# Kernel optimization log

Hardware: AMD Instinct MI355X
Metric: run time of the kernel (lower is better)

The kernel has to match this reference:

```python
import jax, jax.numpy as jnp
import numpy as np

B, C, FRAMES, E, W = 8, 2, 3999, 512, 16
STEP = W // 2  # frame_step = W//2 = 8


def setup_inputs() -> dict:
    key = jax.random.key(0)
    k1, k2 = jax.random.split(key)
    dec_input = jax.random.normal(k1, (B, C, FRAMES, E), dtype=jnp.float32)
    weight = jax.random.normal(k2, (W, E), dtype=jnp.float32) * (1.0 / np.sqrt(E))
    return {"dec_input": dec_input, "weight": weight}


def overlap_and_add(signal, frame_step):
    # signal: [..., frames, frame_length] -> [..., (frames-1)*step + frame_length]
    frames, frame_length = signal.shape[-2], signal.shape[-1]
    output_size = frame_step * (frames - 1) + frame_length
    # target sample index of every element of `signal`
    idx = (jnp.arange(frames)[:, None] * frame_step
           + jnp.arange(frame_length)[None, :]).reshape(-1)  # [frames*frame_length]
    flat = signal.reshape(*signal.shape[:-2], frames * frame_length)
    out = jnp.zeros((*signal.shape[:-2], output_size), dtype=signal.dtype)
    # scatter-accumulate overlapping frames along the last axis
    return out.at[..., idx].add(flat)


def reference(dec_input, weight):
    # dec_input: [B, C, frames, E]; weight: [W, E] (nn.Linear(E, W, bias=False))
    est_source = jnp.einsum('bcle,we->bclw', dec_input, weight)  # [B, C, frames, W]
    return overlap_and_add(est_source, STEP)  # [B, C, T]
```

## Files before the change

kernel.cpp:

```cpp
#include <hip/hip_runtime.h>
#include <cstdint>
#include <cstddef>


#define NBC     16
#define FRAMES  3999
#define EE      512
#define TOUT    32000
#define NGROUP  4000
#define GPB     63

__global__ __launch_bounds__(256, 4) void decoder_kernel(
    const float* __restrict__ dec,
    const float* __restrict__ wgt,
    float* __restrict__ out)
{
    __shared__ float smem[16 * EE];
    float* wl  = smem;
    float* red = smem;

    const int tid   = threadIdx.x;
    const int bc    = blockIdx.x >> 6;
    const int chunk = blockIdx.x & 63;
    const int g0    = chunk * GPB;

    {
        const float4* ws = (const float4*)wgt;
        float4*       wd = (float4*)wl;
        #pragma unroll
        for (int i = 0; i < 8; ++i)
            wd[tid + 256 * i] = ws[tid + 256 * i];
    }
    __syncthreads();

    const int s = tid & 63;
    const int q = tid >> 6;
    const int f = g0 - 1 + s;
    const float vmask = (f >= 0 && f < FRAMES) ? 1.0f : 0.0f;
    const int fr = min(max(f, 0), FRAMES - 1);

    const float* arow = dec + ((size_t)bc * FRAMES + fr) * EE + q * 128;
    const float* wbase = wl + q * 128;

    float acc[16];
    #pragma unroll
    for (int w = 0; w < 16; ++w) acc[w] = 0.f;

    #pragma unroll
    for (int c = 0; c < 8; ++c) {
        float4 xv[4];
        #pragma unroll
        for (int u = 0; u < 4; ++u)
            xv[u] = *(const float4*)(arow + c * 16 + 4 * u);

        #pragma unroll
        for (int w = 0; w < 16; ++w) {
            const float4* wrow = (const float4*)(wbase + w * EE + c * 16);
            float sum = 0.f;
            #pragma unroll
            for (int u = 0; u < 4; ++u) {
                const float4 wq = wrow[u];
                sum += xv[u].x * wq.x + xv[u].y * wq.y
                     + xv[u].z * wq.z + xv[u].w * wq.w;
            }
            acc[w] += sum;
        }
    }

    __syncthreads();
    #pragma unroll
    for (int w = 0; w < 16; ++w)
        red[(q * 16 + w) * 64 + s] = acc[w] * vmask;
    __syncthreads();

    for (int o = tid; o < GPB * 8; o += 256) {
        const int j = o >> 3;
        const int i = o & 7;
        const int g = g0 + j;
        if (g < NGROUP) {
            float v = 0.f;
            #pragma unroll
            for (int qq = 0; qq < 4; ++qq)
                v += red[(qq * 16 + i) * 64 + (j + 1)]
                   + red[(qq * 16 + 8 + i) * 64 + j];
            out[(size_t)bc * TOUT + g * 8 + i] = v;
        }
    }
}

extern "C" void kernel_launch(void* const* d_in, const int* in_sizes, int n_in,
                              void* d_out, int out_size, void* d_ws, size_t ws_size,
                              hipStream_t stream) {
    const float* dec = (const float*)d_in[0];
    const float* wgt = (const float*)d_in[1];
    float* out = (float*)d_out;

    decoder_kernel<<<dim3(1024), dim3(256), 0, stream>>>(dec, wgt, out);
}
```

Measured before the change: 197.5 us.

## Read weights via wave-uniform scalar loads and double-buffer activation loads

Drops the weight copy into shared memory and its barrier. Each wave's weight row offset is made uniform with readfirstlane, so weights can be fetched by scalar loads straight from global memory. Activation float4 loads are double-buffered one chunk ahead to overlap with the FMAs, and the per-row partial sums are folded straight into the accumulators. This cuts LDS traffic and one barrier, but relies on the compiler issuing scalar loads and adds register pressure from the extra buffer.

```diff
diff --git a/kernel.cpp b/kernel.cpp
--- a/kernel.cpp
+++ b/kernel.cpp
@@ -15,59 +15,55 @@
     const float* __restrict__ wgt,
     float* __restrict__ out)
 {
-    __shared__ float smem[16 * EE];
-    float* wl  = smem;
-    float* red = smem;
+    __shared__ float red[4 * 16 * 64];
 
     const int tid   = threadIdx.x;
     const int bc    = blockIdx.x >> 6;
     const int chunk = blockIdx.x & 63;
     const int g0    = chunk * GPB;
 
-    {
-        const float4* ws = (const float4*)wgt;
-        float4*       wd = (float4*)wl;
-        #pragma unroll
-        for (int i = 0; i < 8; ++i)
-            wd[tid + 256 * i] = ws[tid + 256 * i];
-    }
-    __syncthreads();
+    const int s = tid & 63;
+    const int q = __builtin_amdgcn_readfirstlane(tid >> 6);
 
-    const int s = tid & 63;
-    const int q = tid >> 6;
     const int f = g0 - 1 + s;
     const float vmask = (f >= 0 && f < FRAMES) ? 1.0f : 0.0f;
     const int fr = min(max(f, 0), FRAMES - 1);
 
-    const float* arow = dec + ((size_t)bc * FRAMES + fr) * EE + q * 128;
-    const float* wbase = wl + q * 128;
+    const float* arow  = dec + ((size_t)bc * FRAMES + fr) * EE + q * 128;
+    const float* wrow  = wgt + q * 128;
 
     float acc[16];
     #pragma unroll
     for (int w = 0; w < 16; ++w) acc[w] = 0.f;
 
+    float4 xv[2][4];
+    #pragma unroll
+    for (int u = 0; u < 4; ++u)
+        xv[0][u] = *(const float4*)(arow + 4 * u);
+
     #pragma unroll
     for (int c = 0; c < 8; ++c) {
-        float4 xv[4];
-        #pragma unroll
-        for (int u = 0; u < 4; ++u)
-            xv[u] = *(const float4*)(arow + c * 16 + 4 * u);
-
+        const int cur = c & 1;
+        if (c < 7) {
+            #pragma unroll
+            for (int u = 0; u < 4; ++u)
+                xv[cur ^ 1][u] = *(const float4*)(arow + (c + 1) * 16 + 4 * u);
+        }
         #pragma unroll
         for (int w = 0; w < 16; ++w) {
-            const float4* wrow = (const float4*)(wbase + w * EE + c * 16);
-            float sum = 0.f;
+            const float* wr = wrow + w * EE + c * 16;
+            float sum = acc[w];
             #pragma unroll
             for (int u = 0; u < 4; ++u) {
-                const float4 wq = wrow[u];
-                sum += xv[u].x * wq.x + xv[u].y * wq.y
-                     + xv[u].z * wq.z + xv[u].w * wq.w;
+                sum += xv[cur][u].x * wr[4 * u + 0];
+                sum += xv[cur][u].y * wr[4 * u + 1];
+                sum += xv[cur][u].z * wr[4 * u + 2];
+                sum += xv[cur][u].w * wr[4 * u + 3];
             }
-            acc[w] += sum;
+            acc[w] = sum;
         }
     }
 
-    __syncthreads();
     #pragma unroll
     for (int w = 0; w < 16; ++w)
         red[(q * 16 + w) * 64 + s] = acc[w] * vmask;
```

Result: no change. 200.6 us (+1.6%).

## Remap threads so a 16-lane group splits E across one frame, reduce with shuffles

Applied to the files above, without the earlier changes.

Each wave now assigns 16 lanes to cooperatively cover the E dimension of each frame, with 4 frames per thread. Consecutive lanes therefore read consecutive float4s of the input row, giving coalesced global loads, and weight reads from LDS are reused across 4 frames. Partial sums are reduced with xor shuffles instead of a 4-way LDS reduction, and a separate padded reduction buffer replaces the aliased one. The costs are more accumulator registers (64 per thread, with launch bounds relaxed to 3 blocks) and many shuffle instructions in the reduction.

```diff
diff --git a/kernel.cpp b/kernel.cpp
--- a/kernel.cpp
+++ b/kernel.cpp
@@ -9,20 +9,25 @@
 #define TOUT    32000
 #define NGROUP  4000
 #define GPB     63
+#define RSTR    65
 
-__global__ __launch_bounds__(256, 4) void decoder_kernel(
+__global__ __launch_bounds__(256, 3) void decoder_kernel(
     const float* __restrict__ dec,
     const float* __restrict__ wgt,
     float* __restrict__ out)
 {
-    __shared__ float smem[16 * EE];
-    float* wl  = smem;
-    float* red = smem;
+    __shared__ __align__(16) float wl[16 * EE];
+    __shared__ float red[16 * RSTR];
 
     const int tid   = threadIdx.x;
-    const int bc    = blockIdx.x >> 6;
-    const int chunk = blockIdx.x & 63;
+    const int bc    = blockIdx.y;
+    const int chunk = blockIdx.x;
     const int g0    = chunk * GPB;
+
+    const int lane  = tid & 63;
+    const int h     = tid >> 6;
+    const int kappa = lane & 15;
+    const int fg    = lane >> 4;
 
     {
         const float4* ws = (const float4*)wgt;
@@ -33,58 +38,73 @@
     }
     __syncthreads();
 
-    const int s = tid & 63;
-    const int q = tid >> 6;
-    const int f = g0 - 1 + s;
-    const float vmask = (f >= 0 && f < FRAMES) ? 1.0f : 0.0f;
-    const int fr = min(max(f, 0), FRAMES - 1);
+    const float* decb = dec + (size_t)bc * FRAMES * EE;
+    int   slot[4];
+    float msk[4];
+    const float* xp[4];
+    #pragma unroll
+    for (int p = 0; p < 4; ++p) {
+        slot[p] = h * 16 + p * 4 + fg;
+        const int f = g0 - 1 + slot[p];
+        msk[p] = (f >= 0 && f < FRAMES) ? 1.0f : 0.0f;
+        const int fr = min(max(f, 0), FRAMES - 1);
+        xp[p] = decb + (size_t)fr * EE + kappa * 4;
+    }
 
-    const float* arow = dec + ((size_t)bc * FRAMES + fr) * EE + q * 128;
-    const float* wbase = wl + q * 128;
-
-    float acc[16];
+    float acc[4][16];
     #pragma unroll
-    for (int w = 0; w < 16; ++w) acc[w] = 0.f;
+    for (int p = 0; p < 4; ++p)
+        #pragma unroll
+        for (int w = 0; w < 16; ++w) acc[p][w] = 0.f;
 
     #pragma unroll
-    for (int c = 0; c < 8; ++c) {
+    for (int u = 0; u < 8; ++u) {
         float4 xv[4];
         #pragma unroll
-        for (int u = 0; u < 4; ++u)
-            xv[u] = *(const float4*)(arow + c * 16 + 4 * u);
+        for (int p = 0; p < 4; ++p)
+            xv[p] = *(const float4*)(xp[p] + u * 64);
 
         #pragma unroll
-        for (int w = 0; w < 16; ++w) {
-            const float4* wrow = (const float4*)(wbase + w * EE + c * 16);
-            float sum = 0.f;
+        for (int wh = 0; wh < 2; ++wh) {
+            float4 wv[8];
             #pragma unroll
-            for (int u = 0; u < 4; ++u) {
-                const float4 wq = wrow[u];
-                sum += xv[u].x * wq.x + xv[u].y * wq.y
-                     + xv[u].z * wq.z + xv[u].w * wq.w;
-            }
-            acc[w] += sum;
+            for (int w8 = 0; w8 < 8; ++w8)
+                wv[w8] = *(const float4*)(wl + (wh * 8 + w8) * EE
+                                             + u * 64 + kappa * 4);
+            #pragma unroll
+            for (int p = 0; p < 4; ++p)
+                #pragma unroll
+                for (int w8 = 0; w8 < 8; ++w8)
+                    acc[p][wh * 8 + w8] += xv[p].x * wv[w8].x
+                                         + xv[p].y * wv[w8].y
+                                         + xv[p].z * wv[w8].z
+                                         + xv[p].w * wv[w8].w;
         }
     }
 
-    __syncthreads();
     #pragma unroll
-    for (int w = 0; w < 16; ++w)
-        red[(q * 16 + w) * 64 + s] = acc[w] * vmask;
+    for (int p = 0; p < 4; ++p) {
+        #pragma unroll
+        for (int w = 0; w < 16; ++w) {
+            float v = acc[p][w];
+            v += __shfl_xor(v, 1);
+            v += __shfl_xor(v, 2);
+            v += __shfl_xor(v, 4);
+            v += __shfl_xor(v, 8);
+            if (kappa == w)
+                red[w * RSTR + slot[p]] = v * msk[p];
+        }
+    }
     __syncthreads();
 
     for (int o = tid; o < GPB * 8; o += 256) {
         const int j = o >> 3;
         const int i = o & 7;
         const int g = g0 + j;
-        if (g < NGROUP) {
-            float v = 0.f;
-            #pragma unroll
-            for (int qq = 0; qq < 4; ++qq)
-                v += red[(qq * 16 + i) * 64 + (j + 1)]
-                   + red[(qq * 16 + 8 + i) * 64 + j];
-            out[(size_t)bc * TOUT + g * 8 + i] = v;
-        }
+        if (g < NGROUP)
+            out[(size_t)bc * TOUT + g * 8 + i]
+                = red[i * RSTR + (j + 1)]
+                + red[(8 + i) * RSTR + j];
     }
 }
 
@@ -95,5 +115,5 @@
     const float* wgt = (const float*)d_in[1];
     float* out = (float*)d_out;
 
-    decoder_kernel<<<dim3(1024), dim3(256), 0, stream>>>(dec, wgt, out);
+    decoder_kernel<<<dim3(64, 16), dim3(256), 0, stream>>>(dec, wgt, out);
 }
```

Measured after the change: 741.0 us. 3.75x slower.
